# Kernel tuning notes

Hardware: AMD Instinct MI355X
Metric: run time of the kernel (lower is better)

The kernel has to match this reference:

```python
import jax, jax.numpy as jnp
import numpy as np

N, E = 30000, 480000
NFEAT, NHID, H1 = 512, 256, 4


def setup_inputs() -> dict:
    key = jax.random.key(0)
    ks = jax.random.split(key, 16)
    rn = lambda k, shp, sc: jax.random.normal(k, shp, jnp.float32) * sc
    return {
        'x': rn(ks[0], (N, NFEAT), 1.0),
        'edge_index': jax.random.randint(ks[1], (2, E), 0, N),
        # layer 1: in=512, out=256, heads=4, D=64
        'w_kqv1': rn(ks[2], (NFEAT, 3 * NHID), NFEAT ** -0.5),
        'b_kqv1': jnp.zeros((3 * NHID,), jnp.float32),
        'k_rel1': rn(ks[3], (H1, NHID // H1, NHID // H1), (NHID // H1) ** -0.5),
        'v_rel1': rn(ks[4], (H1, NHID // H1, NHID // H1), (NHID // H1) ** -0.5),
        'p_rel1': jnp.ones((H1,), jnp.float32),
        'w_out1': rn(ks[5], (NHID, NHID), NHID ** -0.5),
        'b_out1': jnp.zeros((NHID,), jnp.float32),
        'skip1': jnp.ones((1,), jnp.float32),
        'bn_gamma': jnp.ones((NHID,), jnp.float32),
        'bn_beta': jnp.zeros((NHID,), jnp.float32),
        # layer 2: in=256, out=256, heads=1, D=256
        'w_kqv2': rn(ks[6], (NHID, 3 * NHID), NHID ** -0.5),
        'b_kqv2': jnp.zeros((3 * NHID,), jnp.float32),
        'k_rel2': rn(ks[7], (1, NHID, NHID), NHID ** -0.5),
        'v_rel2': rn(ks[8], (1, NHID, NHID), NHID ** -0.5),
        'p_rel2': jnp.ones((1,), jnp.float32),
        'w_out2': rn(ks[9], (NHID, NHID), NHID ** -0.5),
        'b_out2': jnp.zeros((NHID,), jnp.float32),
        'skip2': jnp.ones((1,), jnp.float32),
    }


def hgt_conv(x, edge_index, w_kqv, b_kqv, k_rel, v_rel, p_rel, w_out, b_out, skip, heads):
    n = x.shape[0]
    out_ch = w_out.shape[0]
    d = out_ch // heads
    kqv = x @ w_kqv + b_kqv                      # [n, 3*out]
    k, q, v = jnp.split(kqv, 3, axis=1)
    k = k.reshape(n, heads, d)
    q = q.reshape(n, heads, d)
    v = v.reshape(n, heads, d)
    # relation-specific per-head transforms of source K/V (single edge type)
    kp = jnp.einsum('nhd,hde->nhe', k, k_rel)
    vp = jnp.einsum('nhd,hde->nhe', v, v_rel)
    src, dst = edge_index[0], edge_index[1]
    # edge-wise attention logits, scaled + relation prior
    alpha = jnp.einsum('ehd,ehd->eh', q[dst], kp[src]) * p_rel / jnp.sqrt(jnp.float32(d))
    # segment softmax over incoming edges of each dst node
    amax = jax.ops.segment_max(alpha, dst, num_segments=n)   # [n, H]
    ex = jnp.exp(alpha - amax[dst])
    denom = jax.ops.segment_sum(ex, dst, num_segments=n) + 1e-16
    a = ex / denom[dst]                                      # [E, H]
    agg = jax.ops.segment_sum(a[:, :, None] * vp[src], dst, num_segments=n)
    out = jax.nn.gelu(agg.reshape(n, out_ch), approximate=False) @ w_out + b_out
    if x.shape[1] == out_ch:  # skip gate only when dims match (PyG HGTConv)
        s = jax.nn.sigmoid(skip)
        out = s * out + (1.0 - s) * x
    return out


def reference(x, edge_index, w_kqv1, b_kqv1, k_rel1, v_rel1, p_rel1, w_out1, b_out1,
              skip1, bn_gamma, bn_beta, w_kqv2, b_kqv2, k_rel2, v_rel2, p_rel2,
              w_out2, b_out2, skip2):
    h = hgt_conv(x, edge_index, w_kqv1, b_kqv1, k_rel1, v_rel1, p_rel1,
                 w_out1, b_out1, skip1, heads=4)
    # BatchNorm1d (training-mode batch stats) + ReLU; dropout is identity (eval)
    mu = h.mean(axis=0)
    var = h.var(axis=0)
    h = (h - mu) / jnp.sqrt(var + 1e-5) * bn_gamma + bn_beta
    h = jax.nn.relu(h)
    out = hgt_conv(h, edge_index, w_kqv2, b_kqv2, k_rel2, v_rel2, p_rel2,
                   w_out2, b_out2, skip2, heads=1)
    return out
```

## Files before the change

kernel.cpp:

```cpp
#include <hip/hip_runtime.h>
#include <math.h>

#define NN 30000
#define NE 480000

typedef _Float16 f16x8 __attribute__((ext_vector_type(8)));
typedef _Float16 f16x4 __attribute__((ext_vector_type(4)));
typedef _Float16 f16x2 __attribute__((ext_vector_type(2)));
typedef float f32x4 __attribute__((ext_vector_type(4)));

__global__ void zero_int_kernel(int* p, int n) {
    int i = blockIdx.x * blockDim.x + threadIdx.x;
    if (i < n) p[i] = 0;
}
__global__ void zero_float_kernel(float* p, int n) {
    int i = blockIdx.x * blockDim.x + threadIdx.x;
    if (i < n) p[i] = 0.0f;
}

__global__ void deg_kernel(const int* __restrict__ dst, int* __restrict__ deg, int e) {
    int i = blockIdx.x * blockDim.x + threadIdx.x;
    if (i < e) atomicAdd(&deg[dst[i]], 1);
}

__global__ __launch_bounds__(1024) void scan_kernel(
    const int* __restrict__ deg, int* __restrict__ row_start,
    int* __restrict__ pos, int n)
{
    __shared__ int smem[1024];
    const int t = threadIdx.x;
    const int base = t * 32;
    int loc[32];
    int s = 0;
#pragma unroll
    for (int g = 0; g < 8; ++g) {
        int idx = base + g * 4;
        int4 d4;
        if (idx + 3 < n) {
            d4 = *(const int4*)(deg + idx);
        } else {
            d4.x = (idx + 0 < n) ? deg[idx + 0] : 0;
            d4.y = (idx + 1 < n) ? deg[idx + 1] : 0;
            d4.z = (idx + 2 < n) ? deg[idx + 2] : 0;
            d4.w = (idx + 3 < n) ? deg[idx + 3] : 0;
        }
        loc[g * 4 + 0] = s; s += d4.x;
        loc[g * 4 + 1] = s; s += d4.y;
        loc[g * 4 + 2] = s; s += d4.z;
        loc[g * 4 + 3] = s; s += d4.w;
    }
    smem[t] = s;
    __syncthreads();
    for (int off = 1; off < 1024; off <<= 1) {
        int tv = 0;
        if (t >= off) tv = smem[t - off];
        __syncthreads();
        smem[t] += tv;
        __syncthreads();
    }
    const int excl = smem[t] - s;
#pragma unroll
    for (int g = 0; g < 32; ++g) {
        int idx = base + g;
        if (idx < n) {
            int r = excl + loc[g];
            row_start[idx] = r;
            pos[idx] = r;
        }
    }
    if (t == 1023) row_start[n] = smem[1023];
}

__global__ void fill_kernel(const int* __restrict__ src, const int* __restrict__ dst,
                            int* __restrict__ pos, int* __restrict__ csr_src, int e) {
    int i = blockIdx.x * blockDim.x + threadIdx.x;
    if (i < e) {
        int p = atomicAdd(&pos[dst[i]], 1);
        csr_src[p] = src[i];
    }
}

__global__ void cvt_f32_f16_kernel(const float* __restrict__ in, _Float16* __restrict__ out, long n8) {
    long i = blockIdx.x * (long)blockDim.x + threadIdx.x;
    if (i >= n8) return;
    float4 a = ((const float4*)in)[2 * i];
    float4 b = ((const float4*)in)[2 * i + 1];
    f16x8 o = {(_Float16)a.x, (_Float16)a.y, (_Float16)a.z, (_Float16)a.w,
               (_Float16)b.x, (_Float16)b.y, (_Float16)b.z, (_Float16)b.w};
    ((f16x8*)out)[i] = o;
}

__global__ void tcvt_kernel(const float* __restrict__ in, _Float16* __restrict__ outT, int K, int N) {
    int n = blockIdx.x * blockDim.x + threadIdx.x;
    int k = blockIdx.y;
    if (n < N) outT[(long)n * K + k] = (_Float16)in[(long)k * N + n];
}

__global__ void bdcvt_kernel(const float* __restrict__ krel, _Float16* __restrict__ outT) {
    int idx = blockIdx.x * blockDim.x + threadIdx.x;
    int e = idx >> 8, d = idx & 255;
    int he = e >> 6, hd = d >> 6;
    float v = (he == hd) ? krel[he * 4096 + (d & 63) * 64 + (e & 63)] : 0.0f;
    outT[idx] = (_Float16)v;
}

__global__ __launch_bounds__(256) void mfma_gemm_kernel(
    const _Float16* __restrict__ A, int lda,
    const _Float16* __restrict__ BT,
    float* __restrict__ Cf,
    _Float16* __restrict__ Ch,
    int ldc, int M, int N, int K,
    const float* __restrict__ bias,
    const float* __restrict__ res,
    const float* __restrict__ skip)
{
    __shared__ __align__(16) _Float16 As[128][40];
    __shared__ __align__(16) _Float16 Bs[128][40];
    const int tid = threadIdx.x;
    const int bm = blockIdx.y * 128, bn = blockIdx.x * 128;
    const int wave = tid >> 6, lane = tid & 63;
    const int wr = wave >> 1, wc = wave & 1;
    const int l16 = lane & 15, quad = lane >> 4;

    f32x4 acc[4][4] = {};

    for (int k0 = 0; k0 < K; k0 += 32) {
#pragma unroll
        for (int c = 0; c < 2; ++c) {
            int chunk = tid + c * 256;
            int row = chunk >> 2, kc = (chunk & 3) << 3;
            f16x8 av = {};
            int gr = bm + row;
            if (gr < M) av = *(const f16x8*)(A + (long)gr * lda + k0 + kc);
            *(f16x8*)&As[row][kc] = av;
            f16x8 bv = {};
            int gn = bn + row;
            if (gn < N) bv = *(const f16x8*)(BT + (long)gn * K + k0 + kc);
            *(f16x8*)&Bs[row][kc] = bv;
        }
        __syncthreads();
        f16x8 af[4], bf[4];
#pragma unroll
        for (int i = 0; i < 4; ++i)
            af[i] = *(const f16x8*)&As[64 * wr + 16 * i + l16][quad * 8];
#pragma unroll
        for (int j = 0; j < 4; ++j)
            bf[j] = *(const f16x8*)&Bs[64 * wc + 16 * j + l16][quad * 8];
#pragma unroll
        for (int i = 0; i < 4; ++i)
#pragma unroll
            for (int j = 0; j < 4; ++j)
                acc[i][j] = __builtin_amdgcn_mfma_f32_16x16x32_f16(af[i], bf[j], acc[i][j], 0, 0, 0);
        __syncthreads();
    }

    float s = 1.0f, om = 0.0f;
    if (skip) {
        float sv = 1.0f / (1.0f + __expf(-skip[0]));
        s = sv; om = 1.0f - sv;
    }
#pragma unroll
    for (int i = 0; i < 4; ++i) {
        int gr0 = bm + 64 * wr + 16 * i + quad * 4;
#pragma unroll
        for (int j = 0; j < 4; ++j) {
            int gc = bn + 64 * wc + 16 * j + l16;
            float bv = bias ? bias[gc] : 0.0f;
#pragma unroll
            for (int r = 0; r < 4; ++r) {
                int row = gr0 + r;
                if (row >= M) continue;
                float v = acc[i][j][r] + bv;
                if (res) v = s * v + om * res[(long)row * ldc + gc];
                if (Cf) Cf[(long)row * ldc + gc] = v;
                if (Ch) Ch[(long)row * ldc + gc] = (_Float16)v;
            }
        }
    }
}

template <int H>
__global__ __launch_bounds__(256) void attn_f16kv_kernel(
    const _Float16* __restrict__ qbase, int ldq,
    const _Float16* __restrict__ kp, const _Float16* __restrict__ vp,
    const float* __restrict__ p_rel,
    const int* __restrict__ row_start, const int* __restrict__ csr_src,
    _Float16* __restrict__ agg, int n)
{
    constexpr int D = 256 / H;
    constexpr int GL = D / 8;
    int node = blockIdx.x * 8 + (threadIdx.x >> 5);
    int l32 = threadIdx.x & 31;
    if (node >= n) return;
    const int head = l32 / GL;
    const float scale = p_rel[head] * rsqrtf((float)D);
    const int ch = l32 * 8;
    f16x8 qv = *(const f16x8*)(qbase + (long)node * ldq + ch);
    f16x2 qp[4];
#pragma unroll
    for (int j = 0; j < 4; ++j) { qp[j][0] = qv[2 * j]; qp[j][1] = qv[2 * j + 1]; }

    const _Float16* kpc = kp + ch;
    const _Float16* vpc = vp + ch;
    int e0 = row_start[node], e1 = row_start[node + 1];
    float m = -1e30f, lsum = 0.0f;
    float a[8] = {};

    int e = e0;
    for (; e + 1 < e1; e += 2) {
        int s0 = csr_src[e], s1 = csr_src[e + 1];
        f16x8 k0 = *(const f16x8*)(kpc + (long)s0 * 256);
        f16x8 k1 = *(const f16x8*)(kpc + (long)s1 * 256);
        f16x8 v0 = *(const f16x8*)(vpc + (long)s0 * 256);
        f16x8 v1 = *(const f16x8*)(vpc + (long)s1 * 256);
        float d0 = 0.0f, d1 = 0.0f;
#pragma unroll
        for (int j = 0; j < 4; ++j) {
            f16x2 k0p = {k0[2 * j], k0[2 * j + 1]};
            f16x2 k1p = {k1[2 * j], k1[2 * j + 1]};
            d0 = __builtin_amdgcn_fdot2(qp[j], k0p, d0, false);
            d1 = __builtin_amdgcn_fdot2(qp[j], k1p, d1, false);
        }
#pragma unroll
        for (int off = 1; off < GL; off <<= 1) {
            d0 += __shfl_xor(d0, off);
            d1 += __shfl_xor(d1, off);
        }
        float al0 = d0 * scale, al1 = d1 * scale;
        float mx = fmaxf(al0, al1);
        float diff = mx - m;
        if (__builtin_expect(diff > 8.0f, 0)) {
            float corr = __expf(-diff);
            lsum *= corr;
#pragma unroll
            for (int j = 0; j < 8; ++j) a[j] *= corr;
            m = mx;
        }
        float w0 = __expf(al0 - m), w1 = __expf(al1 - m);
        lsum += w0 + w1;
#pragma unroll
        for (int j = 0; j < 8; ++j)
            a[j] += w0 * (float)v0[j] + w1 * (float)v1[j];
    }
    if (e < e1) {
        int s0 = csr_src[e];
        f16x8 k0 = *(const f16x8*)(kpc + (long)s0 * 256);
        f16x8 v0 = *(const f16x8*)(vpc + (long)s0 * 256);
        float d0 = 0.0f;
#pragma unroll
        for (int j = 0; j < 4; ++j) {
            f16x2 k0p = {k0[2 * j], k0[2 * j + 1]};
            d0 = __builtin_amdgcn_fdot2(qp[j], k0p, d0, false);
        }
#pragma unroll
        for (int off = 1; off < GL; off <<= 1) d0 += __shfl_xor(d0, off);
        float al0 = d0 * scale;
        float diff = al0 - m;
        if (__builtin_expect(diff > 8.0f, 0)) {
            float corr = __expf(-diff);
            lsum *= corr;
#pragma unroll
            for (int j = 0; j < 8; ++j) a[j] *= corr;
            m = al0;
        }
        float w0 = __expf(al0 - m);
        lsum += w0;
#pragma unroll
        for (int j = 0; j < 8; ++j) a[j] += w0 * (float)v0[j];
    }

    float inv = 1.0f / (lsum + 1e-16f);
    f16x8 o;
#pragma unroll
    for (int j = 0; j < 8; ++j) {
        float v = a[j] * inv;
        v = 0.5f * v * (1.0f + erff(v * 0.70710678118654752f));
        o[j] = (_Float16)v;
    }
    *(f16x8*)(agg + (long)node * 256 + ch) = o;
}

__global__ void bn_stats_kernel(const float* __restrict__ h, float* __restrict__ sums,
                                float* __restrict__ sqs, int n) {
    int c = threadIdx.x;
    float s = 0.f, q = 0.f;
    for (int r = blockIdx.x; r < n; r += gridDim.x) {
        float v = h[(long)r * 256 + c];
        s += v;
        q += v * v;
    }
    atomicAdd(&sums[c], s);
    atomicAdd(&sqs[c], q);
}

__global__ void bn_apply_kernel(float* __restrict__ h, _Float16* __restrict__ oh,
                                const float* __restrict__ sums, const float* __restrict__ sqs,
                                const float* __restrict__ gamma, const float* __restrict__ beta) {
    long idx = blockIdx.x * (long)blockDim.x + threadIdx.x;
    if (idx >= (long)NN * 64) return;
    int cg = (int)(idx & 63) * 4;
    float4 hv = ((float4*)h)[idx];
    float vv[4] = {hv.x, hv.y, hv.z, hv.w};
    const float invn = 1.0f / 30000.0f;
    f16x4 ovh;
#pragma unroll
    for (int r = 0; r < 4; ++r) {
        int c = cg + r;
        float mu = sums[c] * invn;
        float var = sqs[c] * invn - mu * mu;
        float v = (vv[r] - mu) * rsqrtf(var + 1e-5f) * gamma[c] + beta[c];
        v = fmaxf(v, 0.0f);
        vv[r] = v;
        ovh[r] = (_Float16)v;
    }
    ((float4*)h)[idx] = make_float4(vv[0], vv[1], vv[2], vv[3]);
    ((f16x4*)oh)[idx] = ovh;
}

extern "C" void kernel_launch(void* const* d_in, const int* in_sizes, int n_in,
                              void* d_out, int out_size, void* d_ws, size_t ws_size,
                              hipStream_t stream) {
    const float* x       = (const float*)d_in[0];
    const int*   ei      = (const int*)d_in[1];
    const float* w_kqv1  = (const float*)d_in[2];
    const float* b_kqv1  = (const float*)d_in[3];
    const float* k_rel1  = (const float*)d_in[4];
    const float* v_rel1  = (const float*)d_in[5];
    const float* p_rel1  = (const float*)d_in[6];
    const float* w_out1  = (const float*)d_in[7];
    const float* b_out1  = (const float*)d_in[8];
    const float* bn_gamma = (const float*)d_in[10];
    const float* bn_beta  = (const float*)d_in[11];
    const float* w_kqv2  = (const float*)d_in[12];
    const float* b_kqv2  = (const float*)d_in[13];
    const float* k_rel2  = (const float*)d_in[14];
    const float* v_rel2  = (const float*)d_in[15];
    const float* p_rel2  = (const float*)d_in[16];
    const float* w_out2  = (const float*)d_in[17];
    const float* b_out2  = (const float*)d_in[18];
    const float* skip2   = (const float*)d_in[19];
    float* out = (float*)d_out;

    char* p = (char*)d_ws;
    auto alloc = [&](size_t bytes) -> void* {
        void* r = (void*)p;
        p += (bytes + 255) & ~(size_t)255;
        return r;
    };
    _Float16* x_h   = (_Float16*)alloc((size_t)NN * 512 * 2);
    _Float16* kqv_h = (_Float16*)alloc((size_t)NN * 768 * 2);
    _Float16* kp_h  = (_Float16*)alloc((size_t)NN * 256 * 2);
    _Float16* vp_h  = (_Float16*)alloc((size_t)NN * 256 * 2);
    _Float16* agg_h = (_Float16*)alloc((size_t)NN * 256 * 2);
    float* h     = (float*)alloc((size_t)NN * 256 * 4);
    _Float16* hbn_h = (_Float16*)alloc((size_t)NN * 256 * 2);
    _Float16* w1T    = (_Float16*)alloc((size_t)768 * 512 * 2);
    _Float16* bd1k   = (_Float16*)alloc((size_t)256 * 256 * 2);
    _Float16* bd1v   = (_Float16*)alloc((size_t)256 * 256 * 2);
    _Float16* wout1T = (_Float16*)alloc((size_t)256 * 256 * 2);
    _Float16* w2T    = (_Float16*)alloc((size_t)768 * 256 * 2);
    _Float16* krel2T = (_Float16*)alloc((size_t)256 * 256 * 2);
    _Float16* vrel2T = (_Float16*)alloc((size_t)256 * 256 * 2);
    _Float16* wout2T = (_Float16*)alloc((size_t)256 * 256 * 2);
    int*   deg       = (int*)alloc((size_t)NN * 4);
    int*   row_start = (int*)alloc((size_t)(NN + 1) * 4);
    int*   pos       = (int*)alloc((size_t)NN * 4);
    int*   csr_src   = (int*)alloc((size_t)NE * 4);
    float* bnsum     = (float*)alloc(256 * 4);
    float* bnsq      = (float*)alloc(256 * 4);

    const int* esrc = ei;
    const int* edst = ei + NE;

    cvt_f32_f16_kernel<<<(NN * 512 / 8 + 255) / 256, 256, 0, stream>>>(x, x_h, (long)NN * 512 / 8);
    tcvt_kernel<<<dim3(3, 512), 256, 0, stream>>>(w_kqv1, w1T, 512, 768);
    bdcvt_kernel<<<256, 256, 0, stream>>>(k_rel1, bd1k);
    bdcvt_kernel<<<256, 256, 0, stream>>>(v_rel1, bd1v);
    tcvt_kernel<<<dim3(1, 256), 256, 0, stream>>>(w_out1, wout1T, 256, 256);
    tcvt_kernel<<<dim3(3, 256), 256, 0, stream>>>(w_kqv2, w2T, 256, 768);
    tcvt_kernel<<<dim3(1, 256), 256, 0, stream>>>(k_rel2, krel2T, 256, 256);
    tcvt_kernel<<<dim3(1, 256), 256, 0, stream>>>(v_rel2, vrel2T, 256, 256);
    tcvt_kernel<<<dim3(1, 256), 256, 0, stream>>>(w_out2, wout2T, 256, 256);

    zero_int_kernel<<<(NN + 255) / 256, 256, 0, stream>>>(deg, NN);
    deg_kernel<<<(NE + 255) / 256, 256, 0, stream>>>(edst, deg, NE);
    scan_kernel<<<1, 1024, 0, stream>>>(deg, row_start, pos, NN);
    fill_kernel<<<(NE + 255) / 256, 256, 0, stream>>>(esrc, edst, pos, csr_src, NE);

    const int MB = (NN + 127) / 128;

    mfma_gemm_kernel<<<dim3(6, MB), 256, 0, stream>>>(
        x_h, 512, w1T, nullptr, kqv_h, 768, NN, 768, 512, b_kqv1, nullptr, nullptr);
    mfma_gemm_kernel<<<dim3(2, MB), 256, 0, stream>>>(
        kqv_h, 768, bd1k, nullptr, kp_h, 256, NN, 256, 256, nullptr, nullptr, nullptr);
    mfma_gemm_kernel<<<dim3(2, MB), 256, 0, stream>>>(
        kqv_h + 512, 768, bd1v, nullptr, vp_h, 256, NN, 256, 256, nullptr, nullptr, nullptr);
    attn_f16kv_kernel<4><<<(NN + 7) / 8, 256, 0, stream>>>(
        kqv_h + 256, 768, kp_h, vp_h, p_rel1, row_start, csr_src, agg_h, NN);

    mfma_gemm_kernel<<<dim3(2, MB), 256, 0, stream>>>(
        agg_h, 256, wout1T, h, nullptr, 256, NN, 256, 256, b_out1, nullptr, nullptr);

    zero_float_kernel<<<1, 256, 0, stream>>>(bnsum, 256);
    zero_float_kernel<<<1, 256, 0, stream>>>(bnsq, 256);
    bn_stats_kernel<<<256, 256, 0, stream>>>(h, bnsum, bnsq, NN);
    bn_apply_kernel<<<(NN * 64 + 255) / 256, 256, 0, stream>>>(h, hbn_h, bnsum, bnsq, bn_gamma, bn_beta);

    mfma_gemm_kernel<<<dim3(6, MB), 256, 0, stream>>>(
        hbn_h, 256, w2T, nullptr, kqv_h, 768, NN, 768, 256, b_kqv2, nullptr, nullptr);
    mfma_gemm_kernel<<<dim3(2, MB), 256, 0, stream>>>(
        kqv_h, 768, krel2T, nullptr, kp_h, 256, NN, 256, 256, nullptr, nullptr, nullptr);
    mfma_gemm_kernel<<<dim3(2, MB), 256, 0, stream>>>(
        kqv_h + 512, 768, vrel2T, nullptr, vp_h, 256, NN, 256, 256, nullptr, nullptr, nullptr);
    attn_f16kv_kernel<1><<<(NN + 7) / 8, 256, 0, stream>>>(
        kqv_h + 256, 768, kp_h, vp_h, p_rel2, row_start, csr_src, agg_h, NN);

    mfma_gemm_kernel<<<dim3(2, MB), 256, 0, stream>>>(
        agg_h, 256, wout2T, out, nullptr, 256, NN, 256, 256, b_out2, h, skip2);
}
```

Baseline: 720.5 us.

## Fold relation transforms into KQV weights and use direct global-to-LDS loads

Precomputes W_k·k_rel and W_v·v_rel (and the matching biases) on device so the KQV projection directly yields transformed keys and values. This removes four per-node GEMMs and the separate kp/vp buffers, and attention now reads K/V from the strided kqv buffer. The GEMM tile loading switches to global_load_lds with unpadded shared tiles and clamped row indices. Dropping the padding may add LDS bank conflicts, and folding in fp32 before the f16 cast slightly changes rounding.

```diff
diff --git a/kernel.cpp b/kernel.cpp
--- a/kernel.cpp
+++ b/kernel.cpp
@@ -8,6 +8,11 @@
 typedef _Float16 f16x4 __attribute__((ext_vector_type(4)));
 typedef _Float16 f16x2 __attribute__((ext_vector_type(2)));
 typedef float f32x4 __attribute__((ext_vector_type(4)));
+
+#define GLOAD_LDS16(gp, lp)                                        \
+    __builtin_amdgcn_global_load_lds(                              \
+        (const __attribute__((address_space(1))) void*)(gp),       \
+        (__attribute__((address_space(3))) void*)(lp), 16, 0, 0)
 
 __global__ void zero_int_kernel(int* p, int n) {
     int i = blockIdx.x * blockDim.x + threadIdx.x;
@@ -96,12 +101,90 @@
     if (n < N) outT[(long)n * K + k] = (_Float16)in[(long)k * N + n];
 }
 
-__global__ void bdcvt_kernel(const float* __restrict__ krel, _Float16* __restrict__ outT) {
-    int idx = blockIdx.x * blockDim.x + threadIdx.x;
-    int e = idx >> 8, d = idx & 255;
-    int he = e >> 6, hd = d >> 6;
-    float v = (he == hd) ? krel[he * 4096 + (d & 63) * 64 + (e & 63)] : 0.0f;
-    outT[idx] = (_Float16)v;
+__global__ void foldw1_kernel(const float* __restrict__ W,
+                              const float* __restrict__ krel,
+                              const float* __restrict__ vrel,
+                              _Float16* __restrict__ BT) {
+    int k = blockIdx.x * blockDim.x + threadIdx.x;
+    int n = blockIdx.y;
+    if (k >= 512) return;
+    float acc;
+    if (n < 256) {
+        int h = n >> 6, e = n & 63;
+        const float* wr = W + (long)k * 768 + h * 64;
+        const float* kr = krel + h * 4096 + e;
+        acc = 0.f;
+        for (int d = 0; d < 64; ++d) acc += wr[d] * kr[(long)d * 64];
+    } else if (n < 512) {
+        acc = W[(long)k * 768 + n];
+    } else {
+        int m = n - 512, h = m >> 6, e = m & 63;
+        const float* wr = W + (long)k * 768 + 512 + h * 64;
+        const float* vr = vrel + h * 4096 + e;
+        acc = 0.f;
+        for (int d = 0; d < 64; ++d) acc += wr[d] * vr[(long)d * 64];
+    }
+    BT[(long)n * 512 + k] = (_Float16)acc;
+}
+
+__global__ void foldb1_kernel(const float* __restrict__ b, const float* __restrict__ krel,
+                              const float* __restrict__ vrel, float* __restrict__ bf) {
+    int n = blockIdx.x * blockDim.x + threadIdx.x;
+    if (n >= 768) return;
+    float acc;
+    if (n < 256) {
+        int h = n >> 6, e = n & 63;
+        acc = 0.f;
+        for (int d = 0; d < 64; ++d) acc += b[h * 64 + d] * krel[h * 4096 + d * 64 + e];
+    } else if (n < 512) {
+        acc = b[n];
+    } else {
+        int m = n - 512, h = m >> 6, e = m & 63;
+        acc = 0.f;
+        for (int d = 0; d < 64; ++d) acc += b[512 + h * 64 + d] * vrel[h * 4096 + d * 64 + e];
+    }
+    bf[n] = acc;
+}
+
+__global__ void foldw2_kernel(const float* __restrict__ W,
+                              const float* __restrict__ krel2,
+                              const float* __restrict__ vrel2,
+                              _Float16* __restrict__ BT) {
+    int k = blockIdx.x * blockDim.x + threadIdx.x;
+    int n = blockIdx.y;
+    if (k >= 256) return;
+    float acc;
+    if (n < 256) {
+        const float* wr = W + (long)k * 768;
+        const float* kr = krel2 + n;
+        acc = 0.f;
+        for (int d = 0; d < 256; ++d) acc += wr[d] * kr[(long)d * 256];
+    } else if (n < 512) {
+        acc = W[(long)k * 768 + n];
+    } else {
+        const float* wr = W + (long)k * 768 + 512;
+        const float* vr = vrel2 + (n - 512);
+        acc = 0.f;
+        for (int d = 0; d < 256; ++d) acc += wr[d] * vr[(long)d * 256];
+    }
+    BT[(long)n * 256 + k] = (_Float16)acc;
+}
+
+__global__ void foldb2_kernel(const float* __restrict__ b, const float* __restrict__ krel2,
+                              const float* __restrict__ vrel2, float* __restrict__ bf) {
+    int n = blockIdx.x * blockDim.x + threadIdx.x;
+    if (n >= 768) return;
+    float acc;
+    if (n < 256) {
+        acc = 0.f;
+        for (int d = 0; d < 256; ++d) acc += b[d] * krel2[(long)d * 256 + n];
+    } else if (n < 512) {
+        acc = b[n];
+    } else {
+        acc = 0.f;
+        for (int d = 0; d < 256; ++d) acc += b[512 + d] * vrel2[(long)d * 256 + (n - 512)];
+    }
+    bf[n] = acc;
 }
 
 __global__ __launch_bounds__(256) void mfma_gemm_kernel(
@@ -114,30 +197,34 @@
     const float* __restrict__ res,
     const float* __restrict__ skip)
 {
-    __shared__ __align__(16) _Float16 As[128][40];
-    __shared__ __align__(16) _Float16 Bs[128][40];
+    __shared__ __align__(16) _Float16 As[128][32];
+    __shared__ __align__(16) _Float16 Bs[128][32];
     const int tid = threadIdx.x;
     const int bm = blockIdx.y * 128, bn = blockIdx.x * 128;
     const int wave = tid >> 6, lane = tid & 63;
     const int wr = wave >> 1, wc = wave & 1;
     const int l16 = lane & 15, quad = lane >> 4;
 
+    const int r0 = tid >> 2, kc0 = (tid & 3) * 8;
+    const int r1 = r0 + 64;
+    int gra0 = bm + r0; if (gra0 >= M) gra0 = M - 1;
+    int gra1 = bm + r1; if (gra1 >= M) gra1 = M - 1;
+    const _Float16* a0 = A + (long)gra0 * lda + kc0;
+    const _Float16* a1 = A + (long)gra1 * lda + kc0;
+    const _Float16* b0 = BT + (long)(bn + r0) * K + kc0;
+    const _Float16* b1 = BT + (long)(bn + r1) * K + kc0;
+
+    auto ldsA = (__attribute__((address_space(3))) char*)&As[0][0];
+    auto ldsB = (__attribute__((address_space(3))) char*)&Bs[0][0];
+    const int wb = wave * 1024;
+
     f32x4 acc[4][4] = {};
 
     for (int k0 = 0; k0 < K; k0 += 32) {
-#pragma unroll
-        for (int c = 0; c < 2; ++c) {
-            int chunk = tid + c * 256;
-            int row = chunk >> 2, kc = (chunk & 3) << 3;
-            f16x8 av = {};
-            int gr = bm + row;
-            if (gr < M) av = *(const f16x8*)(A + (long)gr * lda + k0 + kc);
-            *(f16x8*)&As[row][kc] = av;
-            f16x8 bv = {};
-            int gn = bn + row;
-            if (gn < N) bv = *(const f16x8*)(BT + (long)gn * K + k0 + kc);
-            *(f16x8*)&Bs[row][kc] = bv;
-        }
+        GLOAD_LDS16(a0 + k0, ldsA + wb);
+        GLOAD_LDS16(a1 + k0, ldsA + 4096 + wb);
+        GLOAD_LDS16(b0 + k0, ldsB + wb);
+        GLOAD_LDS16(b1 + k0, ldsB + 4096 + wb);
         __syncthreads();
         f16x8 af[4], bf[4];
 #pragma unroll
@@ -182,7 +269,7 @@
 template <int H>
 __global__ __launch_bounds__(256) void attn_f16kv_kernel(
     const _Float16* __restrict__ qbase, int ldq,
-    const _Float16* __restrict__ kp, const _Float16* __restrict__ vp,
+    const _Float16* __restrict__ kp, const _Float16* __restrict__ vp, int ldkv,
     const float* __restrict__ p_rel,
     const int* __restrict__ row_start, const int* __restrict__ csr_src,
     _Float16* __restrict__ agg, int n)
@@ -209,10 +296,10 @@
     int e = e0;
     for (; e + 1 < e1; e += 2) {
         int s0 = csr_src[e], s1 = csr_src[e + 1];
-        f16x8 k0 = *(const f16x8*)(kpc + (long)s0 * 256);
-        f16x8 k1 = *(const f16x8*)(kpc + (long)s1 * 256);
-        f16x8 v0 = *(const f16x8*)(vpc + (long)s0 * 256);
-        f16x8 v1 = *(const f16x8*)(vpc + (long)s1 * 256);
+        f16x8 k0 = *(const f16x8*)(kpc + (long)s0 * ldkv);
+        f16x8 k1 = *(const f16x8*)(kpc + (long)s1 * ldkv);
+        f16x8 v0 = *(const f16x8*)(vpc + (long)s0 * ldkv);
+        f16x8 v1 = *(const f16x8*)(vpc + (long)s1 * ldkv);
         float d0 = 0.0f, d1 = 0.0f;
 #pragma unroll
         for (int j = 0; j < 4; ++j) {
@@ -244,8 +331,8 @@
     }
     if (e < e1) {
         int s0 = csr_src[e];
-        f16x8 k0 = *(const f16x8*)(kpc + (long)s0 * 256);
-        f16x8 v0 = *(const f16x8*)(vpc + (long)s0 * 256);
+        f16x8 k0 = *(const f16x8*)(kpc + (long)s0 * ldkv);
+        f16x8 v0 = *(const f16x8*)(vpc + (long)s0 * ldkv);
         float d0 = 0.0f;
 #pragma unroll
         for (int j = 0; j < 4; ++j) {
@@ -349,19 +436,15 @@
     };
     _Float16* x_h   = (_Float16*)alloc((size_t)NN * 512 * 2);
     _Float16* kqv_h = (_Float16*)alloc((size_t)NN * 768 * 2);
-    _Float16* kp_h  = (_Float16*)alloc((size_t)NN * 256 * 2);
-    _Float16* vp_h  = (_Float16*)alloc((size_t)NN * 256 * 2);
     _Float16* agg_h = (_Float16*)alloc((size_t)NN * 256 * 2);
     float* h     = (float*)alloc((size_t)NN * 256 * 4);
     _Float16* hbn_h = (_Float16*)alloc((size_t)NN * 256 * 2);
     _Float16* w1T    = (_Float16*)alloc((size_t)768 * 512 * 2);
-    _Float16* bd1k   = (_Float16*)alloc((size_t)256 * 256 * 2);
-    _Float16* bd1v   = (_Float16*)alloc((size_t)256 * 256 * 2);
     _Float16* wout1T = (_Float16*)alloc((size_t)256 * 256 * 2);
     _Float16* w2T    = (_Float16*)alloc((size_t)768 * 256 * 2);
-    _Float16* krel2T = (_Float16*)alloc((size_t)256 * 256 * 2);
-    _Float16* vrel2T = (_Float16*)alloc((size_t)256 * 256 * 2);
     _Float16* wout2T = (_Float16*)alloc((size_t)256 * 256 * 2);
+    float* bf1       = (float*)alloc(768 * 4);
+    float* bf2       = (float*)alloc(768 * 4);
     int*   deg       = (int*)alloc((size_t)NN * 4);
     int*   row_start = (int*)alloc((size_t)(NN + 1) * 4);
     int*   pos       = (int*)alloc((size_t)NN * 4);
@@ -373,13 +456,11 @@
     const int* edst = ei + NE;
 
     cvt_f32_f16_kernel<<<(NN * 512 / 8 + 255) / 256, 256, 0, stream>>>(x, x_h, (long)NN * 512 / 8);
-    tcvt_kernel<<<dim3(3, 512), 256, 0, stream>>>(w_kqv1, w1T, 512, 768);
-    bdcvt_kernel<<<256, 256, 0, stream>>>(k_rel1, bd1k);
-    bdcvt_kernel<<<256, 256, 0, stream>>>(v_rel1, bd1v);
+    foldw1_kernel<<<dim3(2, 768), 256, 0, stream>>>(w_kqv1, k_rel1, v_rel1, w1T);
+    foldb1_kernel<<<3, 256, 0, stream>>>(b_kqv1, k_rel1, v_rel1, bf1);
     tcvt_kernel<<<dim3(1, 256), 256, 0, stream>>>(w_out1, wout1T, 256, 256);
-    tcvt_kernel<<<dim3(3, 256), 256, 0, stream>>>(w_kqv2, w2T, 256, 768);
-    tcvt_kernel<<<dim3(1, 256), 256, 0, stream>>>(k_rel2, krel2T, 256, 256);
-    tcvt_kernel<<<dim3(1, 256), 256, 0, stream>>>(v_rel2, vrel2T, 256, 256);
+    foldw2_kernel<<<dim3(1, 768), 256, 0, stream>>>(w_kqv2, k_rel2, v_rel2, w2T);
+    foldb2_kernel<<<3, 256, 0, stream>>>(b_kqv2, k_rel2, v_rel2, bf2);
     tcvt_kernel<<<dim3(1, 256), 256, 0, stream>>>(w_out2, wout2T, 256, 256);
 
     zero_int_kernel<<<(NN + 255) / 256, 256, 0, stream>>>(deg, NN);
@@ -390,14 +471,9 @@
     const int MB = (NN + 127) / 128;
 
     mfma_gemm_kernel<<<dim3(6, MB), 256, 0, stream>>>(
-        x_h, 512, w1T, nullptr, kqv_h, 768, NN, 768, 512, b_kqv1, nullptr, nullptr);
-    mfma_gemm_kernel<<<dim3(2, MB), 256, 0, stream>>>(
-        kqv_h, 768, bd1k, nullptr, kp_h, 256, NN, 256, 256, nullptr, nullptr, nullptr);
-    mfma_gemm_kernel<<<dim3(2, MB), 256, 0, stream>>>(
-        kqv_h + 512, 768, bd1v, nullptr, vp_h, 256, NN, 256, 256, nullptr, nullptr, nullptr);
+        x_h, 512, w1T, nullptr, kqv_h, 768, NN, 768, 512, bf1, nullptr, nullptr);
     attn_f16kv_kernel<4><<<(NN + 7) / 8, 256, 0, stream>>>(
-        kqv_h + 256, 768, kp_h, vp_h, p_rel1, row_start, csr_src, agg_h, NN);
-
+        kqv_h + 256, 768, kqv_h, kqv_h + 512, 768, p_rel1, row_start, csr_src, agg_h, NN);
     mfma_gemm_kernel<<<dim3(2, MB), 256, 0, stream>>>(
         agg_h, 256, wout1T, h, nullptr, 256, NN, 256, 256, b_out1, nullptr, nullptr);
 
@@ -407,14 +483,9 @@
     bn_apply_kernel<<<(NN * 64 + 255) / 256, 256, 0, stream>>>(h, hbn_h, bnsum, bnsq, bn_gamma, bn_beta);
 
     mfma_gemm_kernel<<<dim3(6, MB), 256, 0, stream>>>(
-        hbn_h, 256, w2T, nullptr, kqv_h, 768, NN, 768, 256, b_kqv2, nullptr, nullptr);
-    mfma_gemm_kernel<<<dim3(2, MB), 256, 0, stream>>>(
-        kqv_h, 768, krel2T, nullptr, kp_h, 256, NN, 256, 256, nullptr, nullptr, nullptr);
-    mfma_gemm_kernel<<<dim3(2, MB), 256, 0, stream>>>(
-        kqv_h + 512, 768, vrel2T, nullptr, vp_h, 256, NN, 256, 256, nullptr, nullptr, nullptr);
+        hbn_h, 256, w2T, nullptr, kqv_h, 768, NN, 768, 256, bf2, nullptr, nullptr);
     attn_f16kv_kernel<1><<<(NN + 7) / 8, 256, 0, stream>>>(
-        kqv_h + 256, 768, kp_h, vp_h, p_rel2, row_start, csr_src, agg_h, NN);
-
+        kqv_h + 256, 768, kqv_h, kqv_h + 512, 768, p_rel2, row_start, csr_src, agg_h, NN);
     mfma_gemm_kernel<<<dim3(2, MB), 256, 0, stream>>>(
         agg_h, 256, wout2T, out, nullptr, 256, NN, 256, 256, b_out2, h, skip2);
 }
```

Result: faster. 636.8 us (-11.6%).
